# Performance work log

Measured on AMD Instinct MI355X. Metric: run time of the kernel, lower is better.

Reference implementation:

```python
import jax, jax.numpy as jnp
import numpy as np

D_MODEL = 1024
NHEAD = 16
HEAD_DIM = D_MODEL // NHEAD
ROPE_BASE = 10000.0


def rotate_half(x):
    h = x.shape[-1] // 2
    return jnp.concatenate((-x[..., h:], x[..., :h]), axis=-1)


def rope_cos_sin(seq_len, dim, dtype):
    inv_freq = 1.0 / (ROPE_BASE ** (jnp.arange(0, dim, 2, dtype=jnp.float32) / dim))
    t = jnp.arange(seq_len, dtype=jnp.float32)
    freqs = jnp.einsum('i,j->ij', t, inv_freq)  # [S, dim/2]
    emb = jnp.concatenate((freqs, freqs), axis=-1)  # [S, dim]
    return jnp.cos(emb).astype(dtype), jnp.sin(emb).astype(dtype)


def setup_inputs() -> dict:
    key = jax.random.key(0)
    ks = jax.random.split(key, 9)
    b, s = 2, 2048
    lim = 1.0 / np.sqrt(D_MODEL)
    def lin(kw, kb):
        W = jax.random.uniform(kw, (D_MODEL, D_MODEL), jnp.float32, -lim, lim)
        bia = jax.random.uniform(kb, (D_MODEL,), jnp.float32, -lim, lim)
        return W, bia
    Wq, bq = lin(ks[0], ks[1])
    Wk, bk = lin(ks[2], ks[3])
    Wv, bv = lin(ks[4], ks[5])
    Wo, bo = lin(ks[6], ks[7])
    x = jax.random.normal(ks[8], (b, s, D_MODEL), jnp.float32)
    return {"x": x, "Wq": Wq, "bq": bq, "Wk": Wk, "bk": bk,
            "Wv": Wv, "bv": bv, "Wo": Wo, "bo": bo}


def reference(x, Wq, bq, Wk, bk, Wv, bv, Wo, bo):
    b, s, _ = x.shape
    scale = jnp.sqrt(jnp.asarray(HEAD_DIM, x.dtype))
    # projections (torch Linear: y = x @ W.T + b)
    q = x @ Wq.T + bq
    k = x @ Wk.T + bk
    v = x @ Wv.T + bv
    # [b, h, s, d]
    def split_heads(t):
        return t.reshape(b, s, NHEAD, HEAD_DIM).transpose(0, 2, 1, 3)
    q, k, v = split_heads(q), split_heads(k), split_heads(v)
    cos, sin = rope_cos_sin(s, HEAD_DIM, x.dtype)  # [s, d]
    q = q * cos + rotate_half(q) * sin
    k = k * cos + rotate_half(k) * sin
    scores = jnp.einsum('bhqd,bhkd->bhqk', q, k) / scale
    probs = jax.nn.softmax(scores, axis=-1)
    out = jnp.einsum('bhqk,bhkd->bhqd', probs, v)
    out = out.transpose(0, 2, 1, 3).reshape(b, s, D_MODEL)
    return out @ Wo.T + bo
```

## Files before the change

### kernel.cpp

```cpp
#include <hip/hip_runtime.h>
#include <hip/hip_bf16.h>
#include <stdint.h>


typedef __attribute__((ext_vector_type(8))) short bf16x8;
typedef __attribute__((ext_vector_type(4))) float f32x4;
typedef __attribute__((ext_vector_type(16))) float f32x16;
typedef __attribute__((ext_vector_type(4))) short short4v;
typedef __attribute__((ext_vector_type(4))) float float4v;
typedef __attribute__((ext_vector_type(4))) unsigned uint32x4;

#define DEV __device__ __forceinline__

DEV short f2bf(float f) {
  union { float f; uint32_t u; } v; v.f = f;
  uint32_t r = (v.u + 0x7fffu + ((v.u >> 16) & 1u)) >> 16;
  return (short)(uint16_t)r;
}
DEV float bf2f(short b) {
  union { uint32_t u; float f; } v; v.u = ((uint32_t)(uint16_t)b) << 16;
  return v.f;
}
DEV unsigned cvtpk(float a, float b) {
  unsigned d;
  asm("v_cvt_pk_bf16_f32 %0, %1, %2" : "=v"(d) : "v"(a), "v"(b));
  return d;
}
DEV void gload16(const void* g, const void* l) {
  __builtin_amdgcn_global_load_lds((const __attribute__((address_space(1))) void*)g,
                                   (__attribute__((address_space(3))) void*)l, 16, 0, 0);
}

__global__ void convert_kernel(const float* __restrict__ x,
                               const float* __restrict__ wq, const float* __restrict__ wk,
                               const float* __restrict__ wv, const float* __restrict__ wo,
                               short* __restrict__ xb, short* __restrict__ wqb,
                               short* __restrict__ wkb, short* __restrict__ wvb,
                               short* __restrict__ wob) {
  const int idx = blockIdx.x * blockDim.x + threadIdx.x;
  const float* src; short* dst; int off;
  if (idx < 1048576)      { src = x;  dst = xb;  off = idx; }
  else if (idx < 1310720) { src = wq; dst = wqb; off = idx - 1048576; }
  else if (idx < 1572864) { src = wk; dst = wkb; off = idx - 1310720; }
  else if (idx < 1835008) { src = wv; dst = wvb; off = idx - 1572864; }
  else                    { src = wo; dst = wob; off = idx - 1835008; }
  float4v v = *(const float4v*)(src + (size_t)off * 4);
  short4v o;
  o[0] = f2bf(v[0]); o[1] = f2bf(v[1]); o[2] = f2bf(v[2]); o[3] = f2bf(v[3]);
  *(short4v*)(dst + (size_t)off * 4) = o;
}

__global__ void rope_table_kernel(float* __restrict__ ct, float* __restrict__ st) {
  const int idx = blockIdx.x * blockDim.x + threadIdx.x;
  const int t = idx >> 5, j = idx & 31;
  const float f = (float)t * exp2f(-(float)j * (13.287712379549449f / 32.f));
  ct[idx] = cosf(f);
  st[idx] = sinf(f);
}

template<bool FINAL>
__global__ __launch_bounds__(256, 2) void gemm_bt(
    const short* __restrict__ A,
    const short* __restrict__ W0, const short* __restrict__ W1, const short* __restrict__ W2,
    const float* __restrict__ b0, const float* __restrict__ b1, const float* __restrict__ b2,
    short* __restrict__ o0, short* __restrict__ o1, short* __restrict__ o2,
    float* __restrict__ of,
    const float* __restrict__ ct, const float* __restrict__ st) {
  constexpr int K = 1024;
  __shared__ short lds[2 * 128 * 64];
  short* As = lds;
  short* Ws = lds + 128 * 64;

  const int tid = threadIdx.x;
  const int lane = tid & 63;
  const int w = tid >> 6;
  const int wr = w >> 1, wc = w & 1;
  const int bn = blockIdx.x, bm = blockIdx.y, z = blockIdx.z;

  const short* Wt = (z == 0) ? W0 : (z == 1 ? W1 : W2);
  const float* bias = (z == 0) ? b0 : (z == 1 ? b1 : b2);
  short* ob = (z == 0) ? o0 : (z == 1 ? o1 : o2);

  const int lrow = lane >> 3;
  const int clog = 16 * ((lane & 7) ^ lrow);

  f32x4 acc[4][4] = {};
  const size_t arowbase = (size_t)(bm * 128) * K;
  const size_t wrowbase = (size_t)(bn * 128) * K;

  for (int kt = 0; kt < K / 64; ++kt) {
    __syncthreads();
#pragma unroll
    for (int i = 0; i < 4; ++i) {
      const int c = i * 4 + w;
      const int row = c * 8 + lrow;
      gload16(A + arowbase + (size_t)row * K + kt * 64 + (clog >> 1),
              (const char*)As + c * 1024);
      gload16(Wt + wrowbase + (size_t)row * K + kt * 64 + (clog >> 1),
              (const char*)Ws + c * 1024);
    }
    __syncthreads();
#pragma unroll
    for (int kk = 0; kk < 2; ++kk) {
      bf16x8 af[4], bf[4];
      const int kb = (kk * 32 + (lane >> 4) * 8) * 2;
#pragma unroll
      for (int mi = 0; mi < 4; ++mi) {
        const int row = wr * 64 + mi * 16 + (lane & 15);
        af[mi] = *(const bf16x8*)((const char*)As + row * 128 + (kb ^ ((row & 7) << 4)));
      }
#pragma unroll
      for (int ni = 0; ni < 4; ++ni) {
        const int row = wc * 64 + ni * 16 + (lane & 15);
        bf[ni] = *(const bf16x8*)((const char*)Ws + row * 128 + (kb ^ ((row & 7) << 4)));
      }
#pragma unroll
      for (int mi = 0; mi < 4; ++mi)
#pragma unroll
        for (int ni = 0; ni < 4; ++ni)
          acc[mi][ni] = __builtin_amdgcn_mfma_f32_16x16x32_bf16(af[mi], bf[ni], acc[mi][ni], 0, 0, 0);
    }
  }

  float bv[4];
#pragma unroll
  for (int ni = 0; ni < 4; ++ni)
    bv[ni] = bias[bn * 128 + wc * 64 + ni * 16 + (lane & 15)];

#pragma unroll
  for (int mi = 0; mi < 4; ++mi) {
#pragma unroll
    for (int r = 0; r < 4; ++r) {
      const int m = bm * 128 + wr * 64 + mi * 16 + (lane >> 4) * 4 + r;
      float v[4];
#pragma unroll
      for (int ni = 0; ni < 4; ++ni) v[ni] = acc[mi][ni][r] + bv[ni];
      if (!FINAL && z < 2) {
        const int s = m & 2047;
        const float sc = (z == 0) ? 0.18033688011f : 1.0f;
#pragma unroll
        for (int jj = 0; jj < 2; ++jj) {
          const int j = jj * 16 + (lane & 15);
          const float c = ct[s * 32 + j] * sc, sn = st[s * 32 + j] * sc;
          const float a = v[jj], bb = v[jj + 2];
          v[jj]     = a * c - bb * sn;
          v[jj + 2] = bb * c + a * sn;
        }
      }
#pragma unroll
      for (int ni = 0; ni < 4; ++ni) {
        const int n = bn * 128 + wc * 64 + ni * 16 + (lane & 15);
        if (FINAL) {
          of[(size_t)m * 1024 + n] = v[ni];
        } else {
          const int b = m >> 11, s = m & 2047, h = n >> 6, d = n & 63;
          ob[(((size_t)(b * 16 + h)) * 2048 + s) * 64 + d] = f2bf(v[ni]);
        }
      }
    }
  }
}

__global__ void vtrans_kernel(const short* __restrict__ v, short* __restrict__ vt) {
  __shared__ short t[64][72];
  const int bh = blockIdx.x, st0 = blockIdx.y * 64;
  const int tid = threadIdx.x;
#pragma unroll
  for (int i = 0; i < 2; ++i) {
    const int j = i * 256 + tid;
    const int row = j >> 3, c8 = (j & 7) * 8;
    *(bf16x8*)&t[row][c8] = *(const bf16x8*)(v + (((size_t)bh * 2048) + st0 + row) * 64 + c8);
  }
  __syncthreads();
#pragma unroll
  for (int i = 0; i < 2; ++i) {
    const int j = i * 256 + tid;
    const int dd = j >> 3, s8 = (j & 7) * 8;
    const int b16 = s8 & ~15;
    const int hi8 = (s8 >> 3) & 1;
    bf16x8 o;
#pragma unroll
    for (int e = 0; e < 8; ++e)
      o[e] = t[b16 + 4 * hi8 + (e & 3) + 8 * (e >> 2)][dd];
    *(bf16x8*)(vt + (((size_t)bh * 64) + dd) * 2048 + st0 + s8) = o;
  }
}

__global__ __launch_bounds__(256, 2) void attn_kernel(
    const short* __restrict__ q, const short* __restrict__ k,
    const short* __restrict__ vt, short* __restrict__ ao) {
  __shared__ char ldsb[65536];

  const int tid = threadIdx.x, lane = tid & 63, w = tid >> 6;
  const int wg = w & 1, g = w >> 1;
  const int hi = lane >> 5;
  const int bh = blockIdx.x, qt = blockIdx.y;
  const int lrow = lane >> 3;
  const int cshort = 8 * ((lane & 7) ^ lrow);

  const int qrow0 = qt * 128 + wg * 64 + (lane & 31);
  const short* qb = q + ((size_t)bh * 2048 + qrow0) * 64 + hi * 8;
  bf16x8 qf0[4], qf1[4];
#pragma unroll
  for (int m = 0; m < 4; ++m) {
    qf0[m] = *(const bf16x8*)(qb + 16 * m);
    qf1[m] = *(const bf16x8*)(qb + 32 * 64 + 16 * m);
  }

  f32x16 acc0[2] = {}, acc1[2] = {};
  float l0 = 0.f, l1 = 0.f;

  char* gbase = ldsb + g * 32768;
  const size_t kvoff = (size_t)g * 1024;

  const short* kp = k + ((size_t)bh * 2048 + kvoff + (wg * 4) * 8 + lrow) * 64 + cshort;
  const short* vp[4];
#pragma unroll
  for (int i = 0; i < 4; ++i)
    vp[i] = vt + ((size_t)bh * 64 + (wg * 4 + i) * 8 + lrow) * 2048 + kvoff + cshort;

#pragma unroll
  for (int i = 0; i < 4; ++i) {
    gload16(kp + i * 512, gbase + (wg * 4 + i) * 1024);
    gload16(vp[i], gbase + 8192 + (wg * 4 + i) * 1024);
  }
  kp += 4096;
#pragma unroll
  for (int i = 0; i < 4; ++i) vp[i] += 64;
  __syncthreads();

  int cur = 0;
  for (int j = 0; j < 16; ++j) {
    if (j < 15) {
      char* nb = gbase + (cur ^ 1) * 16384;
#pragma unroll
      for (int i = 0; i < 4; ++i) {
        gload16(kp + i * 512, nb + (wg * 4 + i) * 1024);
        gload16(vp[i], nb + 8192 + (wg * 4 + i) * 1024);
      }
      kp += 4096;
#pragma unroll
      for (int i = 0; i < 4; ++i) vp[i] += 64;
    }

    const char* kb_ = gbase + cur * 16384;
    const char* vb_ = kb_ + 8192;

    f32x16 stv0[2] = {}, stv1[2] = {};
#pragma unroll
    for (int m = 0; m < 4; ++m) {
      const int bc = 32 * m + 16 * hi;
#pragma unroll
      for (int t = 0; t < 2; ++t) {
        const int row = t * 32 + (lane & 31);
        bf16x8 kf = *(const bf16x8*)(kb_ + row * 128 + (bc ^ ((row & 7) << 4)));
        stv0[t] = __builtin_amdgcn_mfma_f32_32x32x16_bf16(kf, qf0[m], stv0[t], 0, 0, 0);
        stv1[t] = __builtin_amdgcn_mfma_f32_32x32x16_bf16(kf, qf1[m], stv1[t], 0, 0, 0);
      }
    }

#pragma unroll
    for (int t = 0; t < 2; ++t)
#pragma unroll
      for (int r = 0; r < 16; ++r) {
        const float p0 = __builtin_amdgcn_exp2f(stv0[t][r]);
        const float p1 = __builtin_amdgcn_exp2f(stv1[t][r]);
        stv0[t][r] = p0; l0 += p0;
        stv1[t][r] = p1; l1 += p1;
      }

    uint32x4 pu0[4], pu1[4];
#pragma unroll
    for (int sg = 0; sg < 4; ++sg) {
      const int t = sg >> 1, sl = sg & 1;
#pragma unroll
      for (int jj = 0; jj < 4; ++jj) {
        pu0[sg][jj] = cvtpk(stv0[t][8 * sl + 2 * jj], stv0[t][8 * sl + 2 * jj + 1]);
        pu1[sg][jj] = cvtpk(stv1[t][8 * sl + 2 * jj], stv1[t][8 * sl + 2 * jj + 1]);
      }
    }

#pragma unroll
    for (int sg = 0; sg < 4; ++sg) {
      const int t = sg >> 1, sl = sg & 1;
      const bf16x8 pv0 = __builtin_bit_cast(bf16x8, pu0[sg]);
      const bf16x8 pv1 = __builtin_bit_cast(bf16x8, pu1[sg]);
      const int base = 64 * t + 32 * sl + 16 * hi;
#pragma unroll
      for (int db = 0; db < 2; ++db) {
        const int row = db * 32 + (lane & 31);
        const int sw = (row & 7) << 4;
        bf16x8 vv = *(const bf16x8*)(vb_ + row * 128 + (base ^ sw));
        acc0[db] = __builtin_amdgcn_mfma_f32_32x32x16_bf16(vv, pv0, acc0[db], 0, 0, 0);
        acc1[db] = __builtin_amdgcn_mfma_f32_32x32x16_bf16(vv, pv1, acc1[db], 0, 0, 0);
      }
    }

    __syncthreads();
    cur ^= 1;
  }

  l0 += __shfl_xor(l0, 32);
  l1 += __shfl_xor(l1, 32);

  float* fm0 = (float*)(void*)ldsb + (wg * 2 + 0) * 2112;
  float* fm1 = (float*)(void*)ldsb + (wg * 2 + 1) * 2112;
  if (g == 1) {
    fm0[lane] = l0;
    fm1[lane] = l1;
#pragma unroll
    for (int db = 0; db < 2; ++db)
#pragma unroll
      for (int r = 0; r < 16; ++r) {
        fm0[64 + (db * 16 + r) * 64 + lane] = acc0[db][r];
        fm1[64 + (db * 16 + r) * 64 + lane] = acc1[db][r];
      }
  }
  __syncthreads();

  if (g == 0) {
    const int b = bh >> 4, h = bh & 15;
#pragma unroll
    for (int s = 0; s < 2; ++s) {
      float* fm = s ? fm1 : fm0;
      f32x16* accp = s ? acc1 : acc0;
      const float rl = 1.0f / ((s ? l1 : l0) + fm[lane]);
      const int qrow = qrow0 + 32 * s;
      short* orow = ao + ((size_t)b * 2048 + qrow) * 1024 + h * 64;
#pragma unroll
      for (int db = 0; db < 2; ++db)
#pragma unroll
        for (int gq = 0; gq < 4; ++gq) {
          short4v o;
#pragma unroll
          for (int jj = 0; jj < 4; ++jj) {
            const int r = 4 * gq + jj;
            const float v1 = fm[64 + (db * 16 + r) * 64 + lane];
            o[jj] = f2bf((accp[db][r] + v1) * rl);
          }
          *(short4v*)(orow + db * 32 + 8 * gq + 4 * hi) = o;
        }
    }
  }
}

extern "C" void kernel_launch(void* const* d_in, const int* in_sizes, int n_in,
                              void* d_out, int out_size, void* d_ws, size_t ws_size,
                              hipStream_t stream) {
  const float* x  = (const float*)d_in[0];
  const float* Wq = (const float*)d_in[1];
  const float* bq = (const float*)d_in[2];
  const float* Wk = (const float*)d_in[3];
  const float* bk = (const float*)d_in[4];
  const float* Wv = (const float*)d_in[5];
  const float* bv = (const float*)d_in[6];
  const float* Wo = (const float*)d_in[7];
  const float* bo = (const float*)d_in[8];
  float* out = (float*)d_out;

  char* ws = (char*)d_ws;
  short* xb  = (short*)(ws);
  short* wqb = (short*)(ws + 8388608);
  short* wkb = (short*)(ws + 10485760);
  short* wvb = (short*)(ws + 12582912);
  short* wob = (short*)(ws + 14680064);
  float* ct  = (float*)(ws + 16777216);
  float* st  = (float*)(ws + 17039360);
  short* qb  = (short*)(ws + 17301504);
  short* kb  = (short*)(ws + 25690112);
  short* vb  = (short*)(ws + 34078720);
  short* vtb = (short*)(ws + 42467328);
  short* ab  = (short*)(ws + 50855936);

  convert_kernel<<<dim3(8192), dim3(256), 0, stream>>>(x, Wq, Wk, Wv, Wo, xb, wqb, wkb, wvb, wob);
  rope_table_kernel<<<dim3(256), dim3(256), 0, stream>>>(ct, st);
  gemm_bt<false><<<dim3(8, 32, 3), dim3(256), 0, stream>>>(
      xb, wqb, wkb, wvb, bq, bk, bv, qb, kb, vb, (float*)nullptr, ct, st);
  vtrans_kernel<<<dim3(32, 32), dim3(256), 0, stream>>>(vb, vtb);
  attn_kernel<<<dim3(32, 16), dim3(256), 0, stream>>>(qb, kb, vtb, ab);
  gemm_bt<true><<<dim3(8, 32, 1), dim3(256), 0, stream>>>(
      ab, wob, (short*)nullptr, (short*)nullptr, bo, (float*)nullptr, (float*)nullptr,
      (short*)nullptr, (short*)nullptr, (short*)nullptr, out, ct, st);
}
```

Before: 108.2 us.

## Split attention KV loop across four wave groups with single-buffered tiles

Result: slower. 203.4 us (+87.9%).

```diff
diff --git a/kernel.cpp b/kernel.cpp
--- a/kernel.cpp
+++ b/kernel.cpp
@@ -186,7 +186,7 @@
   }
 }
 
-__global__ __launch_bounds__(256, 2) void attn_kernel(
+__global__ __launch_bounds__(512, 4) void attn_kernel(
     const short* __restrict__ q, const short* __restrict__ k,
     const short* __restrict__ vt, short* __restrict__ ao) {
   __shared__ char ldsb[65536];
@@ -210,8 +210,8 @@
   f32x16 acc0[2] = {}, acc1[2] = {};
   float l0 = 0.f, l1 = 0.f;
 
-  char* gbase = ldsb + g * 32768;
-  const size_t kvoff = (size_t)g * 1024;
+  char* gbase = ldsb + g * 16384;
+  const size_t kvoff = (size_t)g * 512;
 
   const short* kp = k + ((size_t)bh * 2048 + kvoff + (wg * 4) * 8 + lrow) * 64 + cshort;
   const short* vp[4];
@@ -219,32 +219,20 @@
   for (int i = 0; i < 4; ++i)
     vp[i] = vt + ((size_t)bh * 64 + (wg * 4 + i) * 8 + lrow) * 2048 + kvoff + cshort;
 
-#pragma unroll
-  for (int i = 0; i < 4; ++i) {
-    gload16(kp + i * 512, gbase + (wg * 4 + i) * 1024);
-    gload16(vp[i], gbase + 8192 + (wg * 4 + i) * 1024);
-  }
-  kp += 4096;
-#pragma unroll
-  for (int i = 0; i < 4; ++i) vp[i] += 64;
-  __syncthreads();
-
-  int cur = 0;
-  for (int j = 0; j < 16; ++j) {
-    if (j < 15) {
-      char* nb = gbase + (cur ^ 1) * 16384;
-#pragma unroll
-      for (int i = 0; i < 4; ++i) {
-        gload16(kp + i * 512, nb + (wg * 4 + i) * 1024);
-        gload16(vp[i], nb + 8192 + (wg * 4 + i) * 1024);
-      }
-      kp += 4096;
-#pragma unroll
-      for (int i = 0; i < 4; ++i) vp[i] += 64;
-    }
-
-    const char* kb_ = gbase + cur * 16384;
-    const char* vb_ = kb_ + 8192;
+  for (int j = 0; j < 8; ++j) {
+    __syncthreads();
+#pragma unroll
+    for (int i = 0; i < 4; ++i) {
+      gload16(kp + i * 512, gbase + (wg * 4 + i) * 1024);
+      gload16(vp[i], gbase + 8192 + (wg * 4 + i) * 1024);
+    }
+    kp += 4096;
+#pragma unroll
+    for (int i = 0; i < 4; ++i) vp[i] += 64;
+    __syncthreads();
+
+    const char* kb_ = gbase;
+    const char* vb_ = gbase + 8192;
 
     f32x16 stv0[2] = {}, stv1[2] = {};
 #pragma unroll
@@ -295,9 +283,6 @@
         acc1[db] = __builtin_amdgcn_mfma_f32_32x32x16_bf16(vv, pv1, acc1[db], 0, 0, 0);
       }
     }
-
-    __syncthreads();
-    cur ^= 1;
   }
 
   l0 += __shfl_xor(l0, 32);
@@ -305,26 +290,40 @@
 
   float* fm0 = (float*)(void*)ldsb + (wg * 2 + 0) * 2112;
   float* fm1 = (float*)(void*)ldsb + (wg * 2 + 1) * 2112;
-  if (g == 1) {
-    fm0[lane] = l0;
-    fm1[lane] = l1;
-#pragma unroll
-    for (int db = 0; db < 2; ++db)
-#pragma unroll
-      for (int r = 0; r < 16; ++r) {
-        fm0[64 + (db * 16 + r) * 64 + lane] = acc0[db][r];
-        fm1[64 + (db * 16 + r) * 64 + lane] = acc1[db][r];
-      }
-  }
-  __syncthreads();
+#pragma unroll 1
+  for (int src = 1; src < 4; ++src) {
+    __syncthreads();
+    if (g == src) {
+      fm0[lane] = l0;
+      fm1[lane] = l1;
+#pragma unroll
+      for (int db = 0; db < 2; ++db)
+#pragma unroll
+        for (int r = 0; r < 16; ++r) {
+          fm0[64 + (db * 16 + r) * 64 + lane] = acc0[db][r];
+          fm1[64 + (db * 16 + r) * 64 + lane] = acc1[db][r];
+        }
+    }
+    __syncthreads();
+    if (g == 0) {
+      l0 += fm0[lane];
+      l1 += fm1[lane];
+#pragma unroll
+      for (int db = 0; db < 2; ++db)
+#pragma unroll
+        for (int r = 0; r < 16; ++r) {
+          acc0[db][r] += fm0[64 + (db * 16 + r) * 64 + lane];
+          acc1[db][r] += fm1[64 + (db * 16 + r) * 64 + lane];
+        }
+    }
+  }
 
   if (g == 0) {
     const int b = bh >> 4, h = bh & 15;
 #pragma unroll
     for (int s = 0; s < 2; ++s) {
-      float* fm = s ? fm1 : fm0;
       f32x16* accp = s ? acc1 : acc0;
-      const float rl = 1.0f / ((s ? l1 : l0) + fm[lane]);
+      const float rl = 1.0f / (s ? l1 : l0);
       const int qrow = qrow0 + 32 * s;
       short* orow = ao + ((size_t)b * 2048 + qrow) * 1024 + h * 64;
 #pragma unroll
@@ -333,11 +332,8 @@
         for (int gq = 0; gq < 4; ++gq) {
           short4v o;
 #pragma unroll
-          for (int jj = 0; jj < 4; ++jj) {
-            const int r = 4 * gq + jj;
-            const float v1 = fm[64 + (db * 16 + r) * 64 + lane];
-            o[jj] = f2bf((accp[db][r] + v1) * rl);
-          }
+          for (int jj = 0; jj < 4; ++jj)
+            o[jj] = f2bf(accp[db][4 * gq + jj] * rl);
           *(short4v*)(orow + db * 32 + 8 * gq + 4 * hi) = o;
         }
     }
@@ -377,7 +373,7 @@
   gemm_bt<false><<<dim3(8, 32, 3), dim3(256), 0, stream>>>(
       xb, wqb, wkb, wvb, bq, bk, bv, qb, kb, vb, (float*)nullptr, ct, st);
   vtrans_kernel<<<dim3(32, 32), dim3(256), 0, stream>>>(vb, vtb);
-  attn_kernel<<<dim3(32, 16), dim3(256), 0, stream>>>(qb, kb, vtb, ab);
+  attn_kernel<<<dim3(32, 16), dim3(512), 0, stream>>>(qb, kb, vtb, ab);
   gemm_bt<true><<<dim3(8, 32, 1), dim3(256), 0, stream>>>(
       ab, wob, (short*)nullptr, (short*)nullptr, bo, (float*)nullptr, (float*)nullptr,
       (short*)nullptr, (short*)nullptr, (short*)nullptr, out, ct, st);
```
